# Kernel tuning notes

Hardware: AMD Instinct MI355X
Metric: run time of the kernel (lower is better)

The kernel has to match this reference:

```python
import jax, jax.numpy as jnp
import numpy as np

S, V_SHELL, V_GRID = 4, 90, 642   # shells, dirs/shell, grid vertices
B, F_IN, X, Y, Z = 2, 8, 12, 12, 12


def setup_inputs() -> dict:
    key = jax.random.key(0)
    k1, k2 = jax.random.split(key)
    x = jax.random.normal(k1, (B, F_IN, S * V_SHELL, X, Y, Z), dtype=jnp.float32)
    # per-shell interpolation matrices S2SH @ SH2S[:C], shape [S, V_shell, V_grid]
    W = jax.random.normal(k2, (S, V_SHELL, V_GRID), dtype=jnp.float32) * 0.05
    # shells are concatenated in order -> shell_inverse is sorted with equal counts
    shell_inverse = jnp.repeat(jnp.arange(S, dtype=jnp.int64), V_SHELL)
    return {"x": x, "W": W, "shell_inverse": shell_inverse}


def reference(x, W, shell_inverse):
    # x: [B, F, V', X, Y, Z] with V' = S * V_shell, shell_inverse sorted -> static reshape
    b, f, vp, xx, yy, zz = x.shape
    s, vs, vg = W.shape
    xs = x.reshape(b, f, s, vs, xx, yy, zz)  # per-shell gather (contiguous blocks)
    # einsum 'ijklmn,kp->ijplmn' per shell; output channel block i*F:(i+1)*F -> shell-major
    y = jnp.einsum('bfskxyz,skp->bsfpxyz', xs, W)
    return y.reshape(b, s * f, vg, xx, yy, zz)
```

## Files before the change

kernel.cpp:

```cpp
#include <hip/hip_runtime.h>
#include <cstdint>
#include <cstddef>

#define NB 2
#define NF 8
#define NS 4
#define NK 90
#define NP 642
#define NXYZ 1728
#define MT 64
#define PTILES 11
#define NG 108
#define XT_TASKS (64 * NG * 3)
#define WT_TASKS (NS * PTILES * 4 * 3)
#define GEMM_TASKS (64 * 54 * PTILES)

typedef __attribute__((ext_vector_type(8))) __bf16 bf16x8;
typedef __attribute__((ext_vector_type(4))) float f32x4;
typedef __attribute__((ext_vector_type(4))) uint32_t u32x4;

__device__ __forceinline__ uint32_t pack2bf(float a, float b) {
    uint32_t ua = __builtin_bit_cast(uint32_t, a);
    uint32_t ub = __builtin_bit_cast(uint32_t, b);
    ua += 0x7FFFu + ((ua >> 16) & 1u);
    ub += 0x7FFFu + ((ub >> 16) & 1u);
    return (ua >> 16) | (ub & 0xFFFF0000u);
}

__global__ __launch_bounds__(256) void prep_frag(
    const float* __restrict__ x, const float* __restrict__ Wm,
    uint32_t* __restrict__ ws)
{
    const int tid  = (int)threadIdx.x;
    const int lane = tid & 63;
    const int lr = lane & 15, lg = lane >> 4;
    const int task = (int)blockIdx.x * 4 + (tid >> 6);

    float v[8];
    if (task < XT_TASKS) {
        int t = task;
        const int kk = t % 3;   t /= 3;
        const int g  = t % NG;  t /= NG;
        const int e  = t;
        const int s = e & 3, bf = e >> 2;
        const float* src = x + (size_t)bf * (NS * NK * NXYZ)
                             + (size_t)s * (NK * NXYZ) + g * 16 + lr;
        #pragma unroll
        for (int j = 0; j < 8; ++j) {
            const int k = kk * 32 + lg * 8 + j;
            v[j] = (k < NK) ? src[(size_t)k * NXYZ] : 0.f;
        }
    } else {
        int t = task - XT_TASKS;
        const int kk = t % 3;      t /= 3;
        const int ni = t % 4;      t /= 4;
        const int pt = t % PTILES; t /= PTILES;
        const int s  = t;
        const int p = pt * MT + ni * 16 + lr;
        const float* src = Wm + (size_t)s * (NK * NP) + p;
        #pragma unroll
        for (int j = 0; j < 8; ++j) {
            const int k = kk * 32 + lg * 8 + j;
            v[j] = (k < NK && p < NP) ? src[(size_t)k * NP] : 0.f;
        }
    }
    u32x4 u;
    u.x = pack2bf(v[0], v[1]);
    u.y = pack2bf(v[2], v[3]);
    u.z = pack2bf(v[4], v[5]);
    u.w = pack2bf(v[6], v[7]);
    *(u32x4*)((char*)ws + (size_t)task * 1024 + lane * 16) = u;
}

__global__ __launch_bounds__(256, 4) void gemm_frag(
    const uint32_t* __restrict__ ws, float* __restrict__ y)
{
    const int tid  = (int)threadIdx.x;
    const int lane = tid & 63;
    const int lr = lane & 15, lg = lane >> 4;
    int t = (int)blockIdx.x * 4 + (tid >> 6);
    const int pt  = t % PTILES; t /= PTILES;
    const int n32 = t % 54;     t /= 54;
    const int e   = t;
    const int s = e & 3, bf = e >> 2;

    const char* base  = (const char*)ws + (size_t)lane * 16;
    const char* xbase = base + (size_t)((e * NG + n32 * 2) * 3) * 1024;
    const char* abase = base + (size_t)(XT_TASKS + ((s * PTILES + pt) * 4) * 3) * 1024;

    bf16x8 bfr[2][3], afr[4][3];
    #pragma unroll
    for (int mi = 0; mi < 2; ++mi)
        #pragma unroll
        for (int kk = 0; kk < 3; ++kk)
            bfr[mi][kk] = *(const bf16x8*)(xbase + (mi * 3 + kk) * 1024);
    #pragma unroll
    for (int ni = 0; ni < 4; ++ni)
        #pragma unroll
        for (int kk = 0; kk < 3; ++kk)
            afr[ni][kk] = *(const bf16x8*)(abase + (ni * 3 + kk) * 1024);

    f32x4 acc[2][4];
    #pragma unroll
    for (int mi = 0; mi < 2; ++mi)
        #pragma unroll
        for (int ni = 0; ni < 4; ++ni)
            acc[mi][ni] = (f32x4){0.f, 0.f, 0.f, 0.f};

    #pragma unroll
    for (int kk = 0; kk < 3; ++kk)
        #pragma unroll
        for (int mi = 0; mi < 2; ++mi)
            #pragma unroll
            for (int ni = 0; ni < 4; ++ni)
                acc[mi][ni] = __builtin_amdgcn_mfma_f32_16x16x32_bf16(
                    bfr[mi][kk], afr[ni][kk], acc[mi][ni], 0, 0, 0);

    const int b = bf >> 3, f = bf & 7;
    const size_t chan = (size_t)b * (NS * NF) + (size_t)s * NF + f;
    float* ybase = y + chan * ((size_t)NP * NXYZ) + n32 * 32 + lg * 4;
    #pragma unroll
    for (int ni = 0; ni < 4; ++ni) {
        const int p = pt * MT + ni * 16 + lr;
        if (p < NP) {
            float* dst = ybase + (size_t)p * NXYZ;
            *(f32x4*)dst = acc[0][ni];
            *(f32x4*)(dst + 16) = acc[1][ni];
        }
    }
}

#define NT 96
#define NTILES 18
#define KP 96
#define ROWB (KP * 2)

__global__ __launch_bounds__(192, 4) void interp_fallback(
    const float* __restrict__ x, const float* __restrict__ Wm,
    float* __restrict__ y)
{
    __shared__ __align__(16) char As[MT * ROWB];
    __shared__ __align__(16) char Bs[NT * ROWB];

    int blk = (int)blockIdx.x;
    const int nt = blk % NTILES; blk /= NTILES;
    const int f  = blk % NF;     blk /= NF;
    const int s  = blk % NS;     blk /= NS;
    const int b  = blk;
    const int tid = (int)threadIdx.x;
    const int n0 = nt * NT;

    {
        const int c  = tid % NT;
        const int kh = tid / NT;
        const float* xp = x + (((size_t)b * NF + f) * (NS * NK) + (size_t)s * NK) * NXYZ
                            + n0 + c;
        const int cs = (c & 7) << 4;
        #pragma unroll
        for (int kk = 0; kk < 48; kk += 8) {
            const int kb = kh * 48 + kk;
            float v[8];
            #pragma unroll
            for (int j = 0; j < 8; ++j) {
                const int k = kb + j;
                v[j] = (k < NK) ? xp[(size_t)k * NXYZ] : 0.f;
            }
            u32x4 u;
            u.x = pack2bf(v[0], v[1]); u.y = pack2bf(v[2], v[3]);
            u.z = pack2bf(v[4], v[5]); u.w = pack2bf(v[6], v[7]);
            *(u32x4*)(Bs + ((c * ROWB + kb * 2) ^ cs)) = u;
        }
    }

    const int lane = tid & 63;
    const int w  = tid / 64;
    const int lr = lane & 15;
    const int lg = lane >> 4;
    const int ls = (lr & 7) << 4;
    const size_t chan = (size_t)b * (NS * NF) + (size_t)s * NF + f;
    float* ybase = y + chan * ((size_t)NP * NXYZ);
    const int xyzbase = n0 + w * 32 + lg * 4;
    const int ar = tid & 63;
    const int akc = tid >> 6;
    const int ars = (ar & 7) << 4;

    for (int pt = 0; pt < PTILES; ++pt) {
        const int p0 = pt * MT;
        __syncthreads();
        {
            const int p = p0 + ar;
            const bool pv = (p < NP);
            const float* wp = Wm + (size_t)s * NK * NP + p;
            #pragma unroll
            for (int kk = 0; kk < 32; kk += 8) {
                const int kb = akc * 32 + kk;
                float v[8];
                #pragma unroll
                for (int j = 0; j < 8; ++j) {
                    const int k = kb + j;
                    v[j] = (pv && (k < NK)) ? wp[(size_t)k * NP] : 0.f;
                }
                u32x4 u;
                u.x = pack2bf(v[0], v[1]); u.y = pack2bf(v[2], v[3]);
                u.z = pack2bf(v[4], v[5]); u.w = pack2bf(v[6], v[7]);
                *(u32x4*)(As + ((ar * ROWB + kb * 2) ^ ars)) = u;
            }
        }
        __syncthreads();

        f32x4 acc[2][4];
        #pragma unroll
        for (int mi = 0; mi < 2; ++mi)
            #pragma unroll
            for (int ni = 0; ni < 4; ++ni)
                acc[mi][ni] = (f32x4){0.f, 0.f, 0.f, 0.f};

        #pragma unroll
        for (int kk = 0; kk < 3; ++kk) {
            const int kbyte = kk * 64 + lg * 16;
            bf16x8 bxyz[2], ap[4];
            #pragma unroll
            for (int mi = 0; mi < 2; ++mi) {
                const int row = w * 32 + mi * 16 + lr;
                bxyz[mi] = *(const bf16x8*)(Bs + ((row * ROWB + kbyte) ^ ls));
            }
            #pragma unroll
            for (int ni = 0; ni < 4; ++ni) {
                const int row = ni * 16 + lr;
                ap[ni] = *(const bf16x8*)(As + ((row * ROWB + kbyte) ^ ls));
            }
            #pragma unroll
            for (int mi = 0; mi < 2; ++mi)
                #pragma unroll
                for (int ni = 0; ni < 4; ++ni)
                    acc[mi][ni] = __builtin_amdgcn_mfma_f32_16x16x32_bf16(
                        bxyz[mi], ap[ni], acc[mi][ni], 0, 0, 0);
        }

        #pragma unroll
        for (int ni = 0; ni < 4; ++ni) {
            const int p = p0 + ni * 16 + lr;
            if (p < NP) {
                float* dst = ybase + (size_t)p * NXYZ + xyzbase;
                *(f32x4*)dst = acc[0][ni];
                *(f32x4*)(dst + 16) = acc[1][ni];
            }
        }
    }
}

extern "C" void kernel_launch(void* const* d_in, const int* in_sizes, int n_in,
                              void* d_out, int out_size, void* d_ws, size_t ws_size,
                              hipStream_t stream) {
    (void)in_sizes; (void)n_in; (void)out_size;
    const float* x  = (const float*)d_in[0];
    const float* Wm = (const float*)d_in[1];
    float* y = (float*)d_out;

    const size_t ws_need = (size_t)(XT_TASKS + WT_TASKS) * 1024;
    if (ws_size >= ws_need) {
        prep_frag<<<(XT_TASKS + WT_TASKS) / 4, 256, 0, stream>>>(x, Wm, (uint32_t*)d_ws);
        gemm_frag<<<GEMM_TASKS / 4, 256, 0, stream>>>((const uint32_t*)d_ws, y);
    } else {
        interp_fallback<<<NB * NS * NF * NTILES, 192, 0, stream>>>(x, Wm, y);
    }
}
```

Before: 82.11 us.

## Stage GEMM output tiles in LDS for contiguous 768-byte row stores

Replaces the per-wave 32x64 GEMM task with a block-level task covering 192 spatial columns by 64 output directions. Each block loads its W fragments once, computes 12 column groups across 4 waves, and writes the results to a swizzled LDS tile. After a barrier it stores full contiguous rows to global memory. The aim is to turn many scattered 64-byte output writes into coalesced long-row writes, at the cost of 48KB of LDS per block, lower occupancy and an extra barrier.

Measured after the change: 89.29 us. 1.09x slower.

```diff
diff --git a/kernel.cpp b/kernel.cpp
--- a/kernel.cpp
+++ b/kernel.cpp
@@ -11,9 +11,12 @@
 #define MT 64
 #define PTILES 11
 #define NG 108
+#define XSEG 192
+#define GSEG 12
+#define NSEG 9
 #define XT_TASKS (64 * NG * 3)
 #define WT_TASKS (NS * PTILES * 4 * 3)
-#define GEMM_TASKS (64 * 54 * PTILES)
+#define LROW 768
 
 typedef __attribute__((ext_vector_type(8))) __bf16 bf16x8;
 typedef __attribute__((ext_vector_type(4))) float f32x4;
@@ -72,61 +75,69 @@
     *(u32x4*)((char*)ws + (size_t)task * 1024 + lane * 16) = u;
 }
 
-__global__ __launch_bounds__(256, 4) void gemm_frag(
+__global__ __launch_bounds__(256, 3) void gemm_t(
     const uint32_t* __restrict__ ws, float* __restrict__ y)
 {
+    __shared__ __align__(16) char tile[MT * LROW];
+
     const int tid  = (int)threadIdx.x;
     const int lane = tid & 63;
+    const int w    = tid >> 6;
     const int lr = lane & 15, lg = lane >> 4;
-    int t = (int)blockIdx.x * 4 + (tid >> 6);
-    const int pt  = t % PTILES; t /= PTILES;
-    const int n32 = t % 54;     t /= 54;
+
+    int t = (int)blockIdx.x;
+    const int sub = t % PTILES; t /= PTILES;
+    const int seg = t % NSEG;   t /= NSEG;
     const int e   = t;
-    const int s = e & 3, bf = e >> 2;
-
-    const char* base  = (const char*)ws + (size_t)lane * 16;
-    const char* xbase = base + (size_t)((e * NG + n32 * 2) * 3) * 1024;
-    const char* abase = base + (size_t)(XT_TASKS + ((s * PTILES + pt) * 4) * 3) * 1024;
-
-    bf16x8 bfr[2][3], afr[4][3];
+    const int s = e & 3, bfi = e >> 2;
+    const int b = bfi >> 3, f = bfi & 7;
+
+    const char* lbase = (const char*)ws + (size_t)lane * 16;
+
+    const char* ab = lbase
+        + ((size_t)XT_TASKS + (size_t)((s * PTILES + sub) * 4) * 3) * 1024;
+    bf16x8 A[4][3];
     #pragma unroll
-    for (int mi = 0; mi < 2; ++mi)
+    for (int nj = 0; nj < 4; ++nj)
         #pragma unroll
         for (int kk = 0; kk < 3; ++kk)
-            bfr[mi][kk] = *(const bf16x8*)(xbase + (mi * 3 + kk) * 1024);
+            A[nj][kk] = *(const bf16x8*)(ab + (nj * 3 + kk) * 1024);
+
+    const int swz = (lr & 7) << 4;
     #pragma unroll
-    for (int ni = 0; ni < 4; ++ni)
-        #pragma unroll
-        for (int kk = 0; kk < 3; ++kk)
-            afr[ni][kk] = *(const bf16x8*)(abase + (ni * 3 + kk) * 1024);
-
-    f32x4 acc[2][4];
+    for (int gi = 0; gi < 3; ++gi) {
+        const int g_l = w * 3 + gi;
+        const int g   = seg * GSEG + g_l;
+        const char* xb = lbase + (size_t)((e * NG + g) * 3) * 1024;
+        bf16x8 B0 = *(const bf16x8*)(xb);
+        bf16x8 B1 = *(const bf16x8*)(xb + 1024);
+        bf16x8 B2 = *(const bf16x8*)(xb + 2048);
+        #pragma unroll
+        for (int nj = 0; nj < 4; ++nj) {
+            f32x4 acc = (f32x4){0.f, 0.f, 0.f, 0.f};
+            acc = __builtin_amdgcn_mfma_f32_16x16x32_bf16(B0, A[nj][0], acc, 0, 0, 0);
+            acc = __builtin_amdgcn_mfma_f32_16x16x32_bf16(B1, A[nj][1], acc, 0, 0, 0);
+            acc = __builtin_amdgcn_mfma_f32_16x16x32_bf16(B2, A[nj][2], acc, 0, 0, 0);
+            const int byte = (nj * 16 + lr) * LROW + g_l * 64 + lg * 16;
+            *(f32x4*)(tile + (byte ^ swz)) = acc;
+        }
+    }
+
+    __syncthreads();
+
+    const size_t chan = (size_t)b * (NS * NF) + (size_t)s * NF + f;
+    float* ybase = y + chan * ((size_t)NP * NXYZ) + seg * XSEG;
+    const int p0 = sub * MT;
     #pragma unroll
-    for (int mi = 0; mi < 2; ++mi)
-        #pragma unroll
-        for (int ni = 0; ni < 4; ++ni)
-            acc[mi][ni] = (f32x4){0.f, 0.f, 0.f, 0.f};
-
-    #pragma unroll
-    for (int kk = 0; kk < 3; ++kk)
-        #pragma unroll
-        for (int mi = 0; mi < 2; ++mi)
-            #pragma unroll
-            for (int ni = 0; ni < 4; ++ni)
-                acc[mi][ni] = __builtin_amdgcn_mfma_f32_16x16x32_bf16(
-                    bfr[mi][kk], afr[ni][kk], acc[mi][ni], 0, 0, 0);
-
-    const int b = bf >> 3, f = bf & 7;
-    const size_t chan = (size_t)b * (NS * NF) + (size_t)s * NF + f;
-    float* ybase = y + chan * ((size_t)NP * NXYZ) + n32 * 32 + lg * 4;
-    #pragma unroll
-    for (int ni = 0; ni < 4; ++ni) {
-        const int p = pt * MT + ni * 16 + lr;
-        if (p < NP) {
-            float* dst = ybase + (size_t)p * NXYZ;
-            *(f32x4*)dst = acc[0][ni];
-            *(f32x4*)(dst + 16) = acc[1][ni];
-        }
+    for (int pass = 0; pass < 12; ++pass) {
+        const int fq  = tid + pass * 256;
+        const int p_l = fq / 48;
+        const int xq  = fq - p_l * 48;
+        const f32x4 v = *(const f32x4*)(
+            tile + ((p_l * LROW + xq * 16) ^ ((p_l & 7) << 4)));
+        const int p = p0 + p_l;
+        if (p < NP)
+            *(f32x4*)(ybase + (size_t)p * NXYZ + xq * 4) = v;
     }
 }
 
@@ -260,7 +271,7 @@
     const size_t ws_need = (size_t)(XT_TASKS + WT_TASKS) * 1024;
     if (ws_size >= ws_need) {
         prep_frag<<<(XT_TASKS + WT_TASKS) / 4, 256, 0, stream>>>(x, Wm, (uint32_t*)d_ws);
-        gemm_frag<<<GEMM_TASKS / 4, 256, 0, stream>>>((const uint32_t*)d_ws, y);
+        gemm_t<<<64 * NSEG * PTILES, 256, 0, stream>>>((const uint32_t*)d_ws, y);
     } else {
         interp_fallback<<<NB * NS * NF * NTILES, 192, 0, stream>>>(x, Wm, y);
     }
```

## Stage x tiles through swizzled LDS for coalesced bf16 fragment prep

Applied to the files above, without the earlier changes.

The x-fragment preparation now has each block load a 90x192 slab of x with coalesced float4 reads. It converts the slab to bf16 into XOR-swizzled shared memory, then gathers the MFMA fragment layout from LDS. The old version read x with scalar strided loads, one row element per lane. This is meant to cut uncoalesced global traffic in the prep kernel, at the cost of 36KB of LDS per block and a block-level barrier.

Measured after the change: 88.72 us. 1.08x slower.

```diff
diff --git a/kernel.cpp b/kernel.cpp
--- a/kernel.cpp
+++ b/kernel.cpp
@@ -14,6 +14,8 @@
 #define XT_TASKS (64 * NG * 3)
 #define WT_TASKS (NS * PTILES * 4 * 3)
 #define GEMM_TASKS (64 * 54 * PTILES)
+#define XPREP_BLOCKS (64 * 9)
+#define WPREP_BLOCKS (WT_TASKS / 4)
 
 typedef __attribute__((ext_vector_type(8))) __bf16 bf16x8;
 typedef __attribute__((ext_vector_type(4))) float f32x4;
@@ -27,49 +29,80 @@
     return (ua >> 16) | (ub & 0xFFFF0000u);
 }
 
-__global__ __launch_bounds__(256) void prep_frag(
+__global__ __launch_bounds__(256) void prep_frag2(
     const float* __restrict__ x, const float* __restrict__ Wm,
     uint32_t* __restrict__ ws)
 {
     const int tid  = (int)threadIdx.x;
     const int lane = tid & 63;
+    const int w    = tid >> 6;
     const int lr = lane & 15, lg = lane >> 4;
-    const int task = (int)blockIdx.x * 4 + (tid >> 6);
-
-    float v[8];
-    if (task < XT_TASKS) {
+
+    if ((int)blockIdx.x < XPREP_BLOCKS) {
+        __shared__ __align__(16) char lds[96 * 384];
+        const int e   = (int)blockIdx.x / 9;
+        const int seg = (int)blockIdx.x % 9;
+        const float* xe = x + (size_t)e * (NK * NXYZ) + seg * 192;
+
+        for (int i = tid; i < 6 * 48; i += 256) {
+            const int r = 90 + i / 48, c4 = i % 48;
+            *(uint64_t*)(lds + ((r * 384 + c4 * 8) ^ (((r >> 3) & 3) << 5))) = 0ull;
+        }
+        #pragma unroll
+        for (int pass = 0; pass < 17; ++pass) {
+            const int i = tid + pass * 256;
+            if (i < 90 * 48) {
+                const int r = i / 48, c4 = i - r * 48;
+                const f32x4 v = *(const f32x4*)(xe + (size_t)r * NXYZ + c4 * 4);
+                const uint64_t uu = (uint64_t)pack2bf(v.x, v.y)
+                                  | ((uint64_t)pack2bf(v.z, v.w) << 32);
+                *(uint64_t*)(lds + ((r * 384 + c4 * 8) ^ (((r >> 3) & 3) << 5))) = uu;
+            }
+        }
+        __syncthreads();
+        #pragma unroll
+        for (int q = 0; q < 9; ++q) {
+            const int fi  = w * 9 + q;
+            const int g_l = fi / 3, kk = fi % 3;
+            const int c   = g_l * 16 + lr;
+            uint32_t h[8];
+            #pragma unroll
+            for (int j = 0; j < 8; ++j) {
+                const int k = kk * 32 + lg * 8 + j;
+                h[j] = *(const uint16_t*)(
+                    lds + ((k * 384 + c * 2) ^ (((k >> 3) & 3) << 5)));
+            }
+            u32x4 u;
+            u.x = h[0] | (h[1] << 16);
+            u.y = h[2] | (h[3] << 16);
+            u.z = h[4] | (h[5] << 16);
+            u.w = h[6] | (h[7] << 16);
+            const int g = seg * 12 + g_l;
+            *(u32x4*)((char*)ws + ((size_t)((e * NG + g) * 3 + kk)) * 1024
+                      + lane * 16) = u;
+        }
+    } else {
+        const int task = ((int)blockIdx.x - XPREP_BLOCKS) * 4 + w;
         int t = task;
-        const int kk = t % 3;   t /= 3;
-        const int g  = t % NG;  t /= NG;
-        const int e  = t;
-        const int s = e & 3, bf = e >> 2;
-        const float* src = x + (size_t)bf * (NS * NK * NXYZ)
-                             + (size_t)s * (NK * NXYZ) + g * 16 + lr;
-        #pragma unroll
-        for (int j = 0; j < 8; ++j) {
-            const int k = kk * 32 + lg * 8 + j;
-            v[j] = (k < NK) ? src[(size_t)k * NXYZ] : 0.f;
-        }
-    } else {
-        int t = task - XT_TASKS;
         const int kk = t % 3;      t /= 3;
         const int ni = t % 4;      t /= 4;
         const int pt = t % PTILES; t /= PTILES;
         const int s  = t;
         const int p = pt * MT + ni * 16 + lr;
         const float* src = Wm + (size_t)s * (NK * NP) + p;
+        float v[8];
         #pragma unroll
         for (int j = 0; j < 8; ++j) {
             const int k = kk * 32 + lg * 8 + j;
             v[j] = (k < NK && p < NP) ? src[(size_t)k * NP] : 0.f;
         }
-    }
-    u32x4 u;
-    u.x = pack2bf(v[0], v[1]);
-    u.y = pack2bf(v[2], v[3]);
-    u.z = pack2bf(v[4], v[5]);
-    u.w = pack2bf(v[6], v[7]);
-    *(u32x4*)((char*)ws + (size_t)task * 1024 + lane * 16) = u;
+        u32x4 u;
+        u.x = pack2bf(v[0], v[1]);
+        u.y = pack2bf(v[2], v[3]);
+        u.z = pack2bf(v[4], v[5]);
+        u.w = pack2bf(v[6], v[7]);
+        *(u32x4*)((char*)ws + (size_t)(XT_TASKS + task) * 1024 + lane * 16) = u;
+    }
 }
 
 __global__ __launch_bounds__(256, 4) void gemm_frag(
@@ -259,7 +292,8 @@
 
     const size_t ws_need = (size_t)(XT_TASKS + WT_TASKS) * 1024;
     if (ws_size >= ws_need) {
-        prep_frag<<<(XT_TASKS + WT_TASKS) / 4, 256, 0, stream>>>(x, Wm, (uint32_t*)d_ws);
+        prep_frag2<<<XPREP_BLOCKS + WPREP_BLOCKS, 256, 0, stream>>>(
+            x, Wm, (uint32_t*)d_ws);
         gemm_frag<<<GEMM_TASKS / 4, 256, 0, stream>>>((const uint32_t*)d_ws, y);
     } else {
         interp_fallback<<<NB * NS * NF * NTILES, 192, 0, stream>>>(x, Wm, y);
```
